# Optimization experiments

Hardware: AMD Instinct MI355X
Metric: run time of the kernel (lower is better)

The kernel has to match this reference:

```python
import jax, jax.numpy as jnp
import numpy as np

TEMPERATURE = 0.01
VMIN, VMAX = -1.0, 1.0
NUM_VALUES = 256


def setup_inputs() -> dict:
    key = jax.random.key(0)
    k_img, k_cmap = jax.random.split(key)
    image = jax.random.uniform(k_img, (4, 3, 512, 512), dtype=jnp.float32)
    cmap = jax.random.uniform(k_cmap, (NUM_VALUES, 3), dtype=jnp.float32)
    idx = jnp.arange(NUM_VALUES, dtype=jnp.float32)
    v_i = VMIN + (VMAX - VMIN) * idx / (NUM_VALUES - 1)
    return {"image": image, "cmap": cmap, "v_i": v_i}


def reference(image, cmap, v_i):
    # image: (N, 3, H, W) -> (N, H, W, 3)
    img = jnp.transpose(image, (0, 2, 3, 1))
    # squared euclidean distance to each of the 256 colormap colors
    # dist[n,h,w,k] = sum_c (img[n,h,w,c] - cmap[k,c])^2
    diff = img[..., None, :] - cmap  # (N, H, W, K, 3)
    distances = jnp.sum(diff * diff, axis=-1)  # (N, H, W, K)
    weights = jax.nn.softmax(-distances / TEMPERATURE, axis=-1)
    velocities = jnp.einsum('nhwk,k->nhw', weights, v_i)
    return velocities
```

## Files before the change

### kernel.cpp

```cpp
#include <hip/hip_runtime.h>
#include <hip/hip_fp16.h>


typedef __attribute__((ext_vector_type(8))) short short8;
typedef __attribute__((ext_vector_type(8))) _Float16 f16x8;
typedef __attribute__((ext_vector_type(4))) float f32x4;

#define HWSZ 262144
#define NPIX 1048576
#define K2F  144.2695040888963f
#define BIASF 14.0f

static __device__ __forceinline__ unsigned f2bf(float x, float* resid) {
  unsigned u = __builtin_bit_cast(unsigned, x);
  unsigned r = (u + 0x7fffu + ((u >> 16) & 1u)) >> 16;
  if (resid) *resid = x - __builtin_bit_cast(float, r << 16);
  return r;
}
static __device__ __forceinline__ unsigned bfp(unsigned lo, unsigned hi) {
  return (lo & 0xffffu) | (hi << 16);
}
static __device__ __forceinline__ unsigned pkrtz(float a, float b) {
  return __builtin_bit_cast(unsigned, __builtin_amdgcn_cvt_pkrtz(a, b));
}

__global__ __launch_bounds__(512, 8) void rgb2vel_main(
    const float* __restrict__ img, const float* __restrict__ cmap,
    const float* __restrict__ vv, float* __restrict__ out) {
  __shared__ __align__(16) unsigned char sA[128 * 80];
  __shared__ __align__(16) int4 sB4[1024];
  __shared__ __align__(16) int4 sBv4[512];
  const int tid = threadIdx.x;
  const int lane = tid & 63;
  const int warp = tid >> 6;
  const int c = lane & 15;
  const int g = lane >> 4;
  const int pb0 = blockIdx.x * 128;

  if (tid < 256) {
    int k = tid;
    float c0 = cmap[k * 3 + 0], c1 = cmap[k * 3 + 1], c2 = cmap[k * 3 + 2];
    float cc[3] = {c0, c1, c2};
    unsigned H[3], M[3], L[3];
    float r;
#pragma unroll
    for (int ch = 0; ch < 3; ++ch) {
      float x = 2.0f * K2F * cc[ch];
      H[ch] = f2bf(x, &r);
      M[ch] = f2bf(r, &r);
      L[ch] = f2bf(r, nullptr);
    }
    float mcc = BIASF - K2F * (c0 * c0 + c1 * c1 + c2 * c2);
    unsigned mh = f2bf(mcc, &r);
    unsigned mm = f2bf(r, &r);
    unsigned ml = f2bf(r, nullptr);
    const unsigned N1 = 0xBF80u;
    unsigned d[16];
    d[0] = bfp(H[0], H[1]); d[1] = bfp(H[2], H[0]); d[2] = bfp(H[1], H[2]);
    d[3] = bfp(M[0], M[1]); d[4] = bfp(M[2], L[0]); d[5] = bfp(L[1], L[2]);
    d[6] = bfp(M[0], M[1]); d[7] = bfp(M[2], H[0]); d[8] = bfp(H[1], H[2]);
    d[9] = bfp(mh, mm);     d[10] = bfp(ml, N1);    d[11] = bfp(N1, N1);
    d[12] = d[13] = d[14] = d[15] = 0u;
    int col = k & 15, tt = k >> 4;
#pragma unroll
    for (int g2 = 0; g2 < 4; ++g2)
      sB4[tt * 64 + g2 * 16 + col] =
          make_int4((int)d[4 * g2 + 0], (int)d[4 * g2 + 1],
                    (int)d[4 * g2 + 2], (int)d[4 * g2 + 3]);
  }

  {
    int u = tid >> 6, l = tid & 63, cc2 = l & 15, gg = l >> 4;
    int4 q = make_int4(0, 0, 0, 0);
    if (cc2 == 0) {
      q = make_int4(0x3C003C00, 0x3C003C00, 0x3C003C00, 0x3C003C00);
    } else if (cc2 == 1) {
      unsigned hq[4];
#pragma unroll
      for (int jp = 0; jp < 4; ++jp) {
        int j0 = 2 * jp, j1 = 2 * jp + 1;
        int i0 = (2 * u + (j0 >> 2)) * 16 + gg * 4 + (j0 & 3);
        int i1 = (2 * u + (j1 >> 2)) * 16 + gg * 4 + (j1 & 3);
        unsigned h0 = (unsigned)__half_as_ushort(__float2half(vv[i0]));
        unsigned h1 = (unsigned)__half_as_ushort(__float2half(vv[i1]));
        hq[jp] = h0 | (h1 << 16);
      }
      q = make_int4((int)hq[0], (int)hq[1], (int)hq[2], (int)hq[3]);
    }
    sBv4[tid] = q;
  }

  if (tid >= 384) {
    int px = tid & 127;
    int idx = pb0 + px;
    int n = idx >> 18;
    int hw = idx & (HWSZ - 1);
    const float* pbp = img + (size_t)n * 3 * HWSZ + hw;
    float p0 = pbp[0], p1 = pbp[HWSZ], p2 = pbp[2 * HWSZ];
    float pc[3] = {p0, p1, p2};
    unsigned ph[3], pm[3], pl[3];
    float r;
#pragma unroll
    for (int ch = 0; ch < 3; ++ch) {
      ph[ch] = f2bf(pc[ch], &r);
      pm[ch] = f2bf(r, &r);
      pl[ch] = f2bf(r, nullptr);
    }
    float qv = K2F * (p0 * p0 + p1 * p1 + p2 * p2);
    unsigned qh = f2bf(qv, &r);
    unsigned qm = f2bf(r, &r);
    unsigned ql = f2bf(r, nullptr);
    const unsigned ONE = 0x3F80u;
    int4* sb = (int4*)(sA + px * 80);
    sb[0] = make_int4((int)bfp(ph[0], ph[1]), (int)bfp(ph[2], pm[0]),
                      (int)bfp(pm[1], pm[2]), (int)bfp(ph[0], ph[1]));
    sb[1] = make_int4((int)bfp(ph[2], ph[0]), (int)bfp(ph[1], ph[2]),
                      (int)bfp(pm[0], pm[1]), (int)bfp(pm[2], pl[0]));
    sb[2] = make_int4((int)bfp(pl[1], pl[2]), (int)bfp(ONE, ONE),
                      (int)bfp(ONE, qh),      (int)bfp(qm, ql));
    sb[3] = make_int4(0, 0, 0, 0);
  }
  __syncthreads();

  short8 pfr = *(const short8*)(sA + (warp * 16 + c) * 80 + g * 16);

  f32x4 acc = {0.f, 0.f, 0.f, 0.f};
  const f32x4 z = {0.f, 0.f, 0.f, 0.f};

#pragma unroll
  for (int u = 0; u < 8; ++u) {
    short8 ca = __builtin_bit_cast(short8, sB4[(2 * u) * 64 + lane]);
    short8 cb = __builtin_bit_cast(short8, sB4[(2 * u + 1) * 64 + lane]);
    f32x4 d0 = __builtin_amdgcn_mfma_f32_16x16x32_bf16(ca, pfr, z, 0, 0, 0);
    f32x4 d1 = __builtin_amdgcn_mfma_f32_16x16x32_bf16(cb, pfr, z, 0, 0, 0);
    union { unsigned w[4]; f16x8 v8; } wu;
    wu.w[0] = pkrtz(__builtin_amdgcn_exp2f(d0[0]), __builtin_amdgcn_exp2f(d0[1]));
    wu.w[1] = pkrtz(__builtin_amdgcn_exp2f(d0[2]), __builtin_amdgcn_exp2f(d0[3]));
    wu.w[2] = pkrtz(__builtin_amdgcn_exp2f(d1[0]), __builtin_amdgcn_exp2f(d1[1]));
    wu.w[3] = pkrtz(__builtin_amdgcn_exp2f(d1[2]), __builtin_amdgcn_exp2f(d1[3]));
    f16x8 bv = __builtin_bit_cast(f16x8, sBv4[u * 64 + lane]);
    acc = __builtin_amdgcn_mfma_f32_16x16x32_f16(wu.v8, bv, acc, 0, 0, 0);
  }

  float p0 = __shfl_xor(acc[0], 1);
  float p1 = __shfl_xor(acc[1], 1);
  float p2 = __shfl_xor(acc[2], 1);
  float p3 = __shfl_xor(acc[3], 1);
  if (c == 0) {
    float* o = out + pb0 + warp * 16 + g * 4;
    o[0] = p0 / acc[0];
    o[1] = p1 / acc[1];
    o[2] = p2 / acc[2];
    o[3] = p3 / acc[3];
  }
}

extern "C" void kernel_launch(void* const* d_in, const int* in_sizes, int n_in,
                              void* d_out, int out_size, void* d_ws, size_t ws_size,
                              hipStream_t stream) {
  const float* image = (const float*)d_in[0];
  const float* cmap  = (const float*)d_in[1];
  const float* v_i   = (const float*)d_in[2];
  float* out = (float*)d_out;

  rgb2vel_main<<<NPIX / 128, 512, 0, stream>>>(image, cmap, v_i, out);
}
```

Baseline: 100.6 us.

## Process two pixel tiles per warp to amortize colormap setup and loads

Each block now handles 256 pixels instead of 128, so every warp runs two independent MFMA/exp chains that share the colormap fragments loaded from LDS. The per-block colormap and velocity table preparation is amortized over twice as many pixels and half as many blocks are launched. Pixel staging moves to threads 256-511 and uses a 64-byte stride instead of 80 bytes. The cost is higher register pressure per thread and fewer blocks for load balancing.

```diff
diff --git a/kernel.cpp b/kernel.cpp
--- a/kernel.cpp
+++ b/kernel.cpp
@@ -10,6 +10,7 @@
 #define NPIX 1048576
 #define K2F  144.2695040888963f
 #define BIASF 14.0f
+#define PXB  256
 
 static __device__ __forceinline__ unsigned f2bf(float x, float* resid) {
   unsigned u = __builtin_bit_cast(unsigned, x);
@@ -27,7 +28,7 @@
 __global__ __launch_bounds__(512, 8) void rgb2vel_main(
     const float* __restrict__ img, const float* __restrict__ cmap,
     const float* __restrict__ vv, float* __restrict__ out) {
-  __shared__ __align__(16) unsigned char sA[128 * 80];
+  __shared__ __align__(16) int4 sA4[PXB * 4];
   __shared__ __align__(16) int4 sB4[1024];
   __shared__ __align__(16) int4 sBv4[512];
   const int tid = threadIdx.x;
@@ -35,7 +36,7 @@
   const int warp = tid >> 6;
   const int c = lane & 15;
   const int g = lane >> 4;
-  const int pb0 = blockIdx.x * 128;
+  const int pb0 = blockIdx.x * PXB;
 
   if (tid < 256) {
     int k = tid;
@@ -67,6 +68,35 @@
       sB4[tt * 64 + g2 * 16 + col] =
           make_int4((int)d[4 * g2 + 0], (int)d[4 * g2 + 1],
                     (int)d[4 * g2 + 2], (int)d[4 * g2 + 3]);
+  } else {
+    int px = tid - 256;
+    int idx = pb0 + px;
+    int n = idx >> 18;
+    int hw = idx & (HWSZ - 1);
+    const float* pbp = img + (size_t)n * 3 * HWSZ + hw;
+    float p0 = pbp[0], p1 = pbp[HWSZ], p2 = pbp[2 * HWSZ];
+    float pc[3] = {p0, p1, p2};
+    unsigned ph[3], pm[3], pl[3];
+    float r;
+#pragma unroll
+    for (int ch = 0; ch < 3; ++ch) {
+      ph[ch] = f2bf(pc[ch], &r);
+      pm[ch] = f2bf(r, &r);
+      pl[ch] = f2bf(r, nullptr);
+    }
+    float qv = K2F * (p0 * p0 + p1 * p1 + p2 * p2);
+    unsigned qh = f2bf(qv, &r);
+    unsigned qm = f2bf(r, &r);
+    unsigned ql = f2bf(r, nullptr);
+    const unsigned ONE = 0x3F80u;
+    int4* sb = &sA4[px * 4];
+    sb[0] = make_int4((int)bfp(ph[0], ph[1]), (int)bfp(ph[2], pm[0]),
+                      (int)bfp(pm[1], pm[2]), (int)bfp(ph[0], ph[1]));
+    sb[1] = make_int4((int)bfp(ph[2], ph[0]), (int)bfp(ph[1], ph[2]),
+                      (int)bfp(pm[0], pm[1]), (int)bfp(pm[2], pl[0]));
+    sb[2] = make_int4((int)bfp(pl[1], pl[2]), (int)bfp(ONE, ONE),
+                      (int)bfp(ONE, qh),      (int)bfp(qm, ql));
+    sb[3] = make_int4(0, 0, 0, 0);
   }
 
   {
@@ -89,69 +119,56 @@
     }
     sBv4[tid] = q;
   }
-
-  if (tid >= 384) {
-    int px = tid & 127;
-    int idx = pb0 + px;
-    int n = idx >> 18;
-    int hw = idx & (HWSZ - 1);
-    const float* pbp = img + (size_t)n * 3 * HWSZ + hw;
-    float p0 = pbp[0], p1 = pbp[HWSZ], p2 = pbp[2 * HWSZ];
-    float pc[3] = {p0, p1, p2};
-    unsigned ph[3], pm[3], pl[3];
-    float r;
-#pragma unroll
-    for (int ch = 0; ch < 3; ++ch) {
-      ph[ch] = f2bf(pc[ch], &r);
-      pm[ch] = f2bf(r, &r);
-      pl[ch] = f2bf(r, nullptr);
-    }
-    float qv = K2F * (p0 * p0 + p1 * p1 + p2 * p2);
-    unsigned qh = f2bf(qv, &r);
-    unsigned qm = f2bf(r, &r);
-    unsigned ql = f2bf(r, nullptr);
-    const unsigned ONE = 0x3F80u;
-    int4* sb = (int4*)(sA + px * 80);
-    sb[0] = make_int4((int)bfp(ph[0], ph[1]), (int)bfp(ph[2], pm[0]),
-                      (int)bfp(pm[1], pm[2]), (int)bfp(ph[0], ph[1]));
-    sb[1] = make_int4((int)bfp(ph[2], ph[0]), (int)bfp(ph[1], ph[2]),
-                      (int)bfp(pm[0], pm[1]), (int)bfp(pm[2], pl[0]));
-    sb[2] = make_int4((int)bfp(pl[1], pl[2]), (int)bfp(ONE, ONE),
-                      (int)bfp(ONE, qh),      (int)bfp(qm, ql));
-    sb[3] = make_int4(0, 0, 0, 0);
-  }
   __syncthreads();
 
-  short8 pfr = *(const short8*)(sA + (warp * 16 + c) * 80 + g * 16);
+  short8 pfr0 = __builtin_bit_cast(short8, sA4[(warp * 16 + c) * 4 + g]);
+  short8 pfr1 = __builtin_bit_cast(short8, sA4[(128 + warp * 16 + c) * 4 + g]);
 
-  f32x4 acc = {0.f, 0.f, 0.f, 0.f};
+  f32x4 accA = {0.f, 0.f, 0.f, 0.f};
+  f32x4 accB = {0.f, 0.f, 0.f, 0.f};
   const f32x4 z = {0.f, 0.f, 0.f, 0.f};
 
 #pragma unroll
   for (int u = 0; u < 8; ++u) {
     short8 ca = __builtin_bit_cast(short8, sB4[(2 * u) * 64 + lane]);
     short8 cb = __builtin_bit_cast(short8, sB4[(2 * u + 1) * 64 + lane]);
-    f32x4 d0 = __builtin_amdgcn_mfma_f32_16x16x32_bf16(ca, pfr, z, 0, 0, 0);
-    f32x4 d1 = __builtin_amdgcn_mfma_f32_16x16x32_bf16(cb, pfr, z, 0, 0, 0);
-    union { unsigned w[4]; f16x8 v8; } wu;
-    wu.w[0] = pkrtz(__builtin_amdgcn_exp2f(d0[0]), __builtin_amdgcn_exp2f(d0[1]));
-    wu.w[1] = pkrtz(__builtin_amdgcn_exp2f(d0[2]), __builtin_amdgcn_exp2f(d0[3]));
-    wu.w[2] = pkrtz(__builtin_amdgcn_exp2f(d1[0]), __builtin_amdgcn_exp2f(d1[1]));
-    wu.w[3] = pkrtz(__builtin_amdgcn_exp2f(d1[2]), __builtin_amdgcn_exp2f(d1[3]));
+    f32x4 d0a = __builtin_amdgcn_mfma_f32_16x16x32_bf16(ca, pfr0, z, 0, 0, 0);
+    f32x4 d1a = __builtin_amdgcn_mfma_f32_16x16x32_bf16(cb, pfr0, z, 0, 0, 0);
+    f32x4 d0b = __builtin_amdgcn_mfma_f32_16x16x32_bf16(ca, pfr1, z, 0, 0, 0);
+    f32x4 d1b = __builtin_amdgcn_mfma_f32_16x16x32_bf16(cb, pfr1, z, 0, 0, 0);
+    union { unsigned w[4]; f16x8 v8; } wa, wb;
+    wa.w[0] = pkrtz(__builtin_amdgcn_exp2f(d0a[0]), __builtin_amdgcn_exp2f(d0a[1]));
+    wa.w[1] = pkrtz(__builtin_amdgcn_exp2f(d0a[2]), __builtin_amdgcn_exp2f(d0a[3]));
+    wa.w[2] = pkrtz(__builtin_amdgcn_exp2f(d1a[0]), __builtin_amdgcn_exp2f(d1a[1]));
+    wa.w[3] = pkrtz(__builtin_amdgcn_exp2f(d1a[2]), __builtin_amdgcn_exp2f(d1a[3]));
+    wb.w[0] = pkrtz(__builtin_amdgcn_exp2f(d0b[0]), __builtin_amdgcn_exp2f(d0b[1]));
+    wb.w[1] = pkrtz(__builtin_amdgcn_exp2f(d0b[2]), __builtin_amdgcn_exp2f(d0b[3]));
+    wb.w[2] = pkrtz(__builtin_amdgcn_exp2f(d1b[0]), __builtin_amdgcn_exp2f(d1b[1]));
+    wb.w[3] = pkrtz(__builtin_amdgcn_exp2f(d1b[2]), __builtin_amdgcn_exp2f(d1b[3]));
     f16x8 bv = __builtin_bit_cast(f16x8, sBv4[u * 64 + lane]);
-    acc = __builtin_amdgcn_mfma_f32_16x16x32_f16(wu.v8, bv, acc, 0, 0, 0);
+    accA = __builtin_amdgcn_mfma_f32_16x16x32_f16(wa.v8, bv, accA, 0, 0, 0);
+    accB = __builtin_amdgcn_mfma_f32_16x16x32_f16(wb.v8, bv, accB, 0, 0, 0);
   }
 
-  float p0 = __shfl_xor(acc[0], 1);
-  float p1 = __shfl_xor(acc[1], 1);
-  float p2 = __shfl_xor(acc[2], 1);
-  float p3 = __shfl_xor(acc[3], 1);
+  float a0 = __shfl_xor(accA[0], 1);
+  float a1 = __shfl_xor(accA[1], 1);
+  float a2 = __shfl_xor(accA[2], 1);
+  float a3 = __shfl_xor(accA[3], 1);
+  float b0 = __shfl_xor(accB[0], 1);
+  float b1 = __shfl_xor(accB[1], 1);
+  float b2 = __shfl_xor(accB[2], 1);
+  float b3 = __shfl_xor(accB[3], 1);
   if (c == 0) {
-    float* o = out + pb0 + warp * 16 + g * 4;
-    o[0] = p0 / acc[0];
-    o[1] = p1 / acc[1];
-    o[2] = p2 / acc[2];
-    o[3] = p3 / acc[3];
+    float* oA = out + pb0 + warp * 16 + g * 4;
+    oA[0] = a0 / accA[0];
+    oA[1] = a1 / accA[1];
+    oA[2] = a2 / accA[2];
+    oA[3] = a3 / accA[3];
+    float* oB = out + pb0 + 128 + warp * 16 + g * 4;
+    oB[0] = b0 / accB[0];
+    oB[1] = b1 / accB[1];
+    oB[2] = b2 / accB[2];
+    oB[3] = b3 / accB[3];
   }
 }
 
@@ -163,5 +180,5 @@
   const float* v_i   = (const float*)d_in[2];
   float* out = (float*)d_out;
 
-  rgb2vel_main<<<NPIX / 128, 512, 0, stream>>>(image, cmap, v_i, out);
+  rgb2vel_main<<<NPIX / PXB, 512, 0, stream>>>(image, cmap, v_i, out);
 }
```

New measurement: 97.89 us. 1.03x faster.
